# Performance work log

Measured on AMD Instinct MI355X. Metric: run time of the kernel, lower is better.

## Reference

```python
import jax, jax.numpy as jnp
import numpy as np

N_NODES = 50000
N_EDGES = 800000
IN_CH = 64
HID_CH = 128
OUT_CH = 64
N_GRAPHS = 512


def setup_inputs() -> dict:
    key = jax.random.key(0)
    ks = jax.random.split(key, 10)
    x = jax.random.normal(ks[0], (N_NODES, IN_CH), dtype=jnp.float32)
    edge_index = jax.random.randint(ks[1], (2, N_EDGES), 0, N_NODES, dtype=jnp.int64)
    batch = jnp.sort(jax.random.randint(ks[2], (N_NODES,), 0, N_GRAPHS, dtype=jnp.int64))
    s = 1.0 / np.sqrt(IN_CH)
    # SAGEConv (mean aggr): lin_l applied to aggregated neighbors (with bias),
    # lin_r applied to root features (no bias).
    W_l = jax.random.uniform(ks[3], (HID_CH, IN_CH), minval=-s, maxval=s, dtype=jnp.float32)
    b_l = jax.random.uniform(ks[4], (HID_CH,), minval=-s, maxval=s, dtype=jnp.float32)
    W_r = jax.random.uniform(ks[5], (HID_CH, IN_CH), minval=-s, maxval=s, dtype=jnp.float32)
    sh = 1.0 / np.sqrt(HID_CH)
    W_att = jax.random.uniform(ks[6], (1, HID_CH), minval=-sh, maxval=sh, dtype=jnp.float32)
    b_att = jax.random.uniform(ks[7], (1,), minval=-sh, maxval=sh, dtype=jnp.float32)
    W_out = jax.random.uniform(ks[8], (OUT_CH, HID_CH), minval=-sh, maxval=sh, dtype=jnp.float32)
    b_out = jax.random.uniform(ks[9], (OUT_CH,), minval=-sh, maxval=sh, dtype=jnp.float32)
    return {"x": x, "edge_index": edge_index, "batch": batch,
            "W_l": W_l, "b_l": b_l, "W_r": W_r,
            "W_att": W_att, "b_att": b_att, "W_out": W_out, "b_out": b_out}


def reference(x, edge_index, batch, W_l, b_l, W_r, W_att, b_att, W_out, b_out):
    src, dst = edge_index[0], edge_index[1]
    # mean aggregation of neighbor (source) features at each target node
    agg = jax.ops.segment_sum(x[src], dst, num_segments=N_NODES)  # [N, IN]
    deg = jax.ops.segment_sum(jnp.ones((N_EDGES,), x.dtype), dst, num_segments=N_NODES)
    agg = agg / jnp.maximum(deg, 1.0)[:, None]
    # SAGEConv: lin_l(aggr) + lin_r(x), then ReLU
    h = jax.nn.relu(agg @ W_l.T + b_l + x @ W_r.T)  # [N, HID]
    # attention weighting
    scores = jax.nn.sigmoid(h @ W_att.T + b_att)  # [N, 1]
    h = h * scores
    # global mean pool per graph
    pooled = jax.ops.segment_sum(h, batch, num_segments=N_GRAPHS)  # [B, HID]
    counts = jax.ops.segment_sum(jnp.ones((N_NODES,), x.dtype), batch, num_segments=N_GRAPHS)
    pooled = pooled / jnp.maximum(counts, 1.0)[:, None]
    return pooled @ W_out.T + b_out  # [B, OUT]
```

## Files before the change

kernel.cpp:

```cpp
#include <hip/hip_runtime.h>
#include <hip/hip_bf16.h>

#define N_NODES 50000
#define N_EDGES 800000
#define IN_CH 64
#define HID_CH 128
#define OUT_CH 64
#define N_GRAPHS 512
#define CAP 64
#define TN 16
#define NPB 64
#define NSTAGE (NPB / TN)

__device__ __forceinline__ void atomAddF(float* p, float v) {
    unsafeAtomicAdd(p, v);
}

#define PIN4(v) asm volatile("" : "+v"(v.x), "+v"(v.y), "+v"(v.z), "+v"(v.w))


__global__ __launch_bounds__(256) void scatter_pad(
    const int* __restrict__ ei, int* __restrict__ degi,
    unsigned short* __restrict__ csr16)
{
    int e = blockIdx.x * 256 + threadIdx.x;
    if (e >= N_EDGES) return;
    int src = ei[e];
    int dst = ei[N_EDGES + e];
    int pos = atomicAdd(&degi[dst], 1);
    csr16[(dst << 6) + pos] = (unsigned short)src;
}

__global__ __launch_bounds__(256) void gather_kernel(
    const float* __restrict__ x, const unsigned short* __restrict__ csr16,
    const int* __restrict__ degi, float* __restrict__ agg)
{
    int wid  = (blockIdx.x * 256 + threadIdx.x) >> 6;
    int lane = threadIdx.x & 63;
    if (wid >= N_NODES) return;
    int d = degi[wid];
    const unsigned short* b = csr16 + ((size_t)wid << 6);
    int g  = lane >> 4;
    int c4 = lane & 15;
    float4 acc  = make_float4(0.f, 0.f, 0.f, 0.f);
    float4 acc2 = make_float4(0.f, 0.f, 0.f, 0.f);
    int i = g;
    for (; i + 4 < d; i += 8) {
        int s0 = b[i];
        int s1 = b[i + 4];
        float4 v0 = *reinterpret_cast<const float4*>(x + (size_t)s0 * IN_CH + c4 * 4);
        float4 v1 = *reinterpret_cast<const float4*>(x + (size_t)s1 * IN_CH + c4 * 4);
        acc.x  += v0.x; acc.y  += v0.y; acc.z  += v0.z; acc.w  += v0.w;
        acc2.x += v1.x; acc2.y += v1.y; acc2.z += v1.z; acc2.w += v1.w;
    }
    if (i < d) {
        int s0 = b[i];
        float4 v0 = *reinterpret_cast<const float4*>(x + (size_t)s0 * IN_CH + c4 * 4);
        acc.x += v0.x; acc.y += v0.y; acc.z += v0.z; acc.w += v0.w;
    }
    acc.x += acc2.x; acc.y += acc2.y; acc.z += acc2.z; acc.w += acc2.w;
    acc.x += __shfl_xor(acc.x, 16); acc.y += __shfl_xor(acc.y, 16);
    acc.z += __shfl_xor(acc.z, 16); acc.w += __shfl_xor(acc.w, 16);
    acc.x += __shfl_xor(acc.x, 32); acc.y += __shfl_xor(acc.y, 32);
    acc.z += __shfl_xor(acc.z, 32); acc.w += __shfl_xor(acc.w, 32);
    if (g == 0) {
        float inv = 1.0f / fmaxf((float)d, 1.0f);
        acc.x *= inv; acc.y *= inv; acc.z *= inv; acc.w *= inv;
        *reinterpret_cast<float4*>(agg + (size_t)wid * IN_CH + c4 * 4) = acc;
    }
}

__global__ __launch_bounds__(256, 4) void node_kernel(
    const float* __restrict__ x, const float* __restrict__ agg,
    const int* __restrict__ batch,
    const float* __restrict__ Wl, const float* __restrict__ bl,
    const float* __restrict__ Wr, const float* __restrict__ Watt,
    const float* __restrict__ batt,
    float* __restrict__ pooled, float* __restrict__ counts)
{
    const int t    = threadIdx.x;
    const int jp   = t & 31;
    const int q    = t >> 5;
    const int w    = t >> 6;
    const int lane = t & 63;

    float4 wrk[4][2], wlk[4][2];
#pragma unroll
    for (int k = 0; k < 4; ++k) {
#pragma unroll
        for (int h = 0; h < 2; ++h) {
            wrk[k][h] = *reinterpret_cast<const float4*>(
                Wr + (size_t)(jp + 32 * k) * IN_CH + q * 8 + h * 4);
            wlk[k][h] = *reinterpret_cast<const float4*>(
                Wl + (size_t)(jp + 32 * k) * IN_CH + q * 8 + h * 4);
            PIN4(wrk[k][h]);
            PIN4(wlk[k][h]);
        }
    }
    const int jj    = t & 127;
    const float blj = bl[jj];
    const float wa  = Watt[jj];
    const float ba  = batt[0];

    __shared__ __align__(16) float4 feat[TN][32];
    float* sh = reinterpret_cast<float*>(feat);
    __shared__ float psum[4][TN][HID_CH];
    __shared__ float sred[2][TN];
    __shared__ float ss[TN];

    float accp = 0.f, cnt = 0.f;
    const int nb0 = blockIdx.x * NPB;
    int curb = batch[nb0];

    for (int s = 0; s < NSTAGE; ++s) {
        const int nb = nb0 + s * TN;
        if (nb >= N_NODES) break;
        __syncthreads();
#pragma unroll
        for (int k = 0; k < 2; ++k) {
            int f    = t + k * 256;
            int node = nb + (f >> 5);
            int slot = f & 31;
            const float* src = (slot < 16)
                ? x   + (size_t)node * IN_CH + slot * 4
                : agg + (size_t)node * IN_CH + (slot - 16) * 4;
            feat[f >> 5][slot] = *reinterpret_cast<const float4*>(src);
        }
        __syncthreads();

#pragma unroll
        for (int n = 0; n < TN; ++n) {
            float4 x0 = feat[n][2 * q];
            float4 x1 = feat[n][2 * q + 1];
            float4 a0 = feat[n][16 + 2 * q];
            float4 a1 = feat[n][16 + 2 * q + 1];
            float p[4];
#pragma unroll
            for (int k = 0; k < 4; ++k) {
                float e0 = wrk[k][0].x * x0.x + wrk[k][0].y * x0.y
                         + wrk[k][0].z * x0.z + wrk[k][0].w * x0.w;
                float e1 = wrk[k][1].x * x1.x + wrk[k][1].y * x1.y
                         + wrk[k][1].z * x1.z + wrk[k][1].w * x1.w;
                float e2 = wlk[k][0].x * a0.x + wlk[k][0].y * a0.y
                         + wlk[k][0].z * a0.z + wlk[k][0].w * a0.w;
                float e3 = wlk[k][1].x * a1.x + wlk[k][1].y * a1.y
                         + wlk[k][1].z * a1.z + wlk[k][1].w * a1.w;
                p[k] = (e0 + e1) + (e2 + e3);
            }
#pragma unroll
            for (int k = 0; k < 4; ++k)
                p[k] += __shfl_xor(p[k], 32);
            if (lane < 32) {
                psum[w][n][jp]      = p[0];
                psum[w][n][jp + 32] = p[1];
                psum[w][n][jp + 64] = p[2];
                psum[w][n][jp + 96] = p[3];
            }
        }
        __syncthreads();

        if (t < 128) {
#pragma unroll
            for (int n = 0; n < TN; ++n) {
                float h = psum[0][n][jj] + psum[1][n][jj]
                        + psum[2][n][jj] + psum[3][n][jj] + blj;
                h = fmaxf(h, 0.f);
                sh[n * HID_CH + jj] = h;
                float r = wa * h;
                r += __shfl_xor(r, 1);  r += __shfl_xor(r, 2);
                r += __shfl_xor(r, 4);  r += __shfl_xor(r, 8);
                r += __shfl_xor(r, 16); r += __shfl_xor(r, 32);
                if (lane == n) sred[t >> 6][n] = r;
            }
        }
        __syncthreads();
        if (t < TN) ss[t] = 1.f / (1.f + expf(-(sred[0][t] + sred[1][t] + ba)));
        __syncthreads();

        if (t < 128) {
#pragma unroll
            for (int n = 0; n < TN; ++n) {
                float hs = sh[n * HID_CH + jj] * ss[n];
                int b = batch[nb + n];
                if (b != curb) {
                    atomAddF(&pooled[(size_t)curb * HID_CH + jj], accp);
                    if (jj == 0) atomAddF(&counts[curb], cnt);
                    accp = 0.f; cnt = 0.f; curb = b;
                }
                accp += hs;
                cnt  += 1.f;
            }
        }
    }
    if (t < 128) {
        atomAddF(&pooled[(size_t)curb * HID_CH + jj], accp);
        if (jj == 0) atomAddF(&counts[curb], cnt);
    }
}

__global__ __launch_bounds__(64) void out_kernel(
    const float* __restrict__ pooled, const float* __restrict__ counts,
    const float* __restrict__ Wout, const float* __restrict__ bout,
    float* __restrict__ out)
{
    const int g = blockIdx.x;
    const int j = threadIdx.x;
    __shared__ __align__(16) float sp[HID_CH];
    float inv = 1.0f / fmaxf(counts[g], 1.0f);
    sp[j]      = pooled[(size_t)g * HID_CH + j] * inv;
    sp[j + 64] = pooled[(size_t)g * HID_CH + 64 + j] * inv;
    __syncthreads();
    float acc = bout[j];
#pragma unroll
    for (int c4 = 0; c4 < HID_CH / 4; ++c4) {
        float4 w = *reinterpret_cast<const float4*>(Wout + (size_t)j * HID_CH + c4 * 4);
        acc += w.x * sp[c4 * 4 + 0] + w.y * sp[c4 * 4 + 1]
             + w.z * sp[c4 * 4 + 2] + w.w * sp[c4 * 4 + 3];
    }
    out[(size_t)g * OUT_CH + j] = acc;
}

extern "C" void kernel_launch(void* const* d_in, const int* in_sizes, int n_in,
                              void* d_out, int out_size, void* d_ws, size_t ws_size,
                              hipStream_t stream)
{
    const float* x     = (const float*)d_in[0];
    const int*   ei    = (const int*)d_in[1];
    const int*   batch = (const int*)d_in[2];
    const float* Wl    = (const float*)d_in[3];
    const float* bl    = (const float*)d_in[4];
    const float* Wr    = (const float*)d_in[5];
    const float* Watt  = (const float*)d_in[6];
    const float* batt  = (const float*)d_in[7];
    const float* Wout  = (const float*)d_in[8];
    const float* bout  = (const float*)d_in[9];
    float* out = (float*)d_out;

    int*            degi   = (int*)d_ws;
    float*          pooled = (float*)(degi + N_NODES);
    float*          counts = pooled + (size_t)N_GRAPHS * HID_CH;
    unsigned short* csr16  = (unsigned short*)(counts + N_GRAPHS);
    float*          agg    = (float*)(csr16 + (size_t)N_NODES * CAP);

    size_t zero_bytes = ((size_t)N_NODES
                       + (size_t)N_GRAPHS * HID_CH + N_GRAPHS) * sizeof(int);
    hipMemsetAsync(d_ws, 0, zero_bytes, stream);

    scatter_pad<<<(N_EDGES + 255) / 256, 256, 0, stream>>>(ei, degi, csr16);
    gather_kernel<<<(N_NODES * 64 + 255) / 256, 256, 0, stream>>>(x, csr16, degi, agg);
    node_kernel<<<(N_NODES + NPB - 1) / NPB, 256, 0, stream>>>(
        x, agg, batch, Wl, bl, Wr, Watt, batt, pooled, counts);
    out_kernel<<<N_GRAPHS, 64, 0, stream>>>(pooled, counts, Wout, bout, out);
}
```

Baseline: 251.3 us.

## Remap node-kernel weight tiling, unroll gather 4-way, and double nodes per block

```diff
diff --git a/kernel.cpp b/kernel.cpp
--- a/kernel.cpp
+++ b/kernel.cpp
@@ -9,14 +9,12 @@
 #define N_GRAPHS 512
 #define CAP 64
 #define TN 16
-#define NPB 64
+#define NPB 128
 #define NSTAGE (NPB / TN)
 
 __device__ __forceinline__ void atomAddF(float* p, float v) {
     unsafeAtomicAdd(p, v);
 }
-
-#define PIN4(v) asm volatile("" : "+v"(v.x), "+v"(v.y), "+v"(v.z), "+v"(v.w))
 
 
 __global__ __launch_bounds__(256) void scatter_pad(
@@ -42,31 +40,44 @@
     const unsigned short* b = csr16 + ((size_t)wid << 6);
     int g  = lane >> 4;
     int c4 = lane & 15;
-    float4 acc  = make_float4(0.f, 0.f, 0.f, 0.f);
-    float4 acc2 = make_float4(0.f, 0.f, 0.f, 0.f);
+    float4 a0 = make_float4(0.f, 0.f, 0.f, 0.f);
+    float4 a1 = make_float4(0.f, 0.f, 0.f, 0.f);
+    float4 a2 = make_float4(0.f, 0.f, 0.f, 0.f);
+    float4 a3 = make_float4(0.f, 0.f, 0.f, 0.f);
     int i = g;
-    for (; i + 4 < d; i += 8) {
-        int s0 = b[i];
-        int s1 = b[i + 4];
+    for (; i + 12 < d; i += 16) {
+        int s0 = b[i], s1 = b[i + 4], s2 = b[i + 8], s3 = b[i + 12];
         float4 v0 = *reinterpret_cast<const float4*>(x + (size_t)s0 * IN_CH + c4 * 4);
         float4 v1 = *reinterpret_cast<const float4*>(x + (size_t)s1 * IN_CH + c4 * 4);
-        acc.x  += v0.x; acc.y  += v0.y; acc.z  += v0.z; acc.w  += v0.w;
-        acc2.x += v1.x; acc2.y += v1.y; acc2.z += v1.z; acc2.w += v1.w;
+        float4 v2 = *reinterpret_cast<const float4*>(x + (size_t)s2 * IN_CH + c4 * 4);
+        float4 v3 = *reinterpret_cast<const float4*>(x + (size_t)s3 * IN_CH + c4 * 4);
+        a0.x += v0.x; a0.y += v0.y; a0.z += v0.z; a0.w += v0.w;
+        a1.x += v1.x; a1.y += v1.y; a1.z += v1.z; a1.w += v1.w;
+        a2.x += v2.x; a2.y += v2.y; a2.z += v2.z; a2.w += v2.w;
+        a3.x += v3.x; a3.y += v3.y; a3.z += v3.z; a3.w += v3.w;
+    }
+    for (; i + 4 < d; i += 8) {
+        int s0 = b[i], s1 = b[i + 4];
+        float4 v0 = *reinterpret_cast<const float4*>(x + (size_t)s0 * IN_CH + c4 * 4);
+        float4 v1 = *reinterpret_cast<const float4*>(x + (size_t)s1 * IN_CH + c4 * 4);
+        a0.x += v0.x; a0.y += v0.y; a0.z += v0.z; a0.w += v0.w;
+        a1.x += v1.x; a1.y += v1.y; a1.z += v1.z; a1.w += v1.w;
     }
     if (i < d) {
         int s0 = b[i];
         float4 v0 = *reinterpret_cast<const float4*>(x + (size_t)s0 * IN_CH + c4 * 4);
-        acc.x += v0.x; acc.y += v0.y; acc.z += v0.z; acc.w += v0.w;
-    }
-    acc.x += acc2.x; acc.y += acc2.y; acc.z += acc2.z; acc.w += acc2.w;
-    acc.x += __shfl_xor(acc.x, 16); acc.y += __shfl_xor(acc.y, 16);
-    acc.z += __shfl_xor(acc.z, 16); acc.w += __shfl_xor(acc.w, 16);
-    acc.x += __shfl_xor(acc.x, 32); acc.y += __shfl_xor(acc.y, 32);
-    acc.z += __shfl_xor(acc.z, 32); acc.w += __shfl_xor(acc.w, 32);
+        a0.x += v0.x; a0.y += v0.y; a0.z += v0.z; a0.w += v0.w;
+    }
+    a0.x += a1.x + a2.x + a3.x; a0.y += a1.y + a2.y + a3.y;
+    a0.z += a1.z + a2.z + a3.z; a0.w += a1.w + a2.w + a3.w;
+    a0.x += __shfl_xor(a0.x, 16); a0.y += __shfl_xor(a0.y, 16);
+    a0.z += __shfl_xor(a0.z, 16); a0.w += __shfl_xor(a0.w, 16);
+    a0.x += __shfl_xor(a0.x, 32); a0.y += __shfl_xor(a0.y, 32);
+    a0.z += __shfl_xor(a0.z, 32); a0.w += __shfl_xor(a0.w, 32);
     if (g == 0) {
         float inv = 1.0f / fmaxf((float)d, 1.0f);
-        acc.x *= inv; acc.y *= inv; acc.z *= inv; acc.w *= inv;
-        *reinterpret_cast<float4*>(agg + (size_t)wid * IN_CH + c4 * 4) = acc;
+        a0.x *= inv; a0.y *= inv; a0.z *= inv; a0.w *= inv;
+        *reinterpret_cast<float4*>(agg + (size_t)wid * IN_CH + c4 * 4) = a0;
     }
 }
 
@@ -79,23 +90,17 @@
     float* __restrict__ pooled, float* __restrict__ counts)
 {
     const int t    = threadIdx.x;
-    const int jp   = t & 31;
-    const int q    = t >> 5;
-    const int w    = t >> 6;
+    const int jp   = t & 63;
+    const int q    = t >> 6;
     const int lane = t & 63;
 
-    float4 wrk[4][2], wlk[4][2];
-#pragma unroll
-    for (int k = 0; k < 4; ++k) {
-#pragma unroll
-        for (int h = 0; h < 2; ++h) {
-            wrk[k][h] = *reinterpret_cast<const float4*>(
-                Wr + (size_t)(jp + 32 * k) * IN_CH + q * 8 + h * 4);
-            wlk[k][h] = *reinterpret_cast<const float4*>(
-                Wl + (size_t)(jp + 32 * k) * IN_CH + q * 8 + h * 4);
-            PIN4(wrk[k][h]);
-            PIN4(wlk[k][h]);
-        }
+    float4 wl0[4], wl1[4], wr0[4], wr1[4];
+#pragma unroll
+    for (int c = 0; c < 4; ++c) {
+        wl0[c] = *reinterpret_cast<const float4*>(Wl + (size_t)jp * IN_CH + q * 16 + c * 4);
+        wr0[c] = *reinterpret_cast<const float4*>(Wr + (size_t)jp * IN_CH + q * 16 + c * 4);
+        wl1[c] = *reinterpret_cast<const float4*>(Wl + (size_t)(jp + 64) * IN_CH + q * 16 + c * 4);
+        wr1[c] = *reinterpret_cast<const float4*>(Wr + (size_t)(jp + 64) * IN_CH + q * 16 + c * 4);
     }
     const int jj    = t & 127;
     const float blj = bl[jj];
@@ -130,32 +135,22 @@
 
 #pragma unroll
         for (int n = 0; n < TN; ++n) {
-            float4 x0 = feat[n][2 * q];
-            float4 x1 = feat[n][2 * q + 1];
-            float4 a0 = feat[n][16 + 2 * q];
-            float4 a1 = feat[n][16 + 2 * q + 1];
-            float p[4];
-#pragma unroll
-            for (int k = 0; k < 4; ++k) {
-                float e0 = wrk[k][0].x * x0.x + wrk[k][0].y * x0.y
-                         + wrk[k][0].z * x0.z + wrk[k][0].w * x0.w;
-                float e1 = wrk[k][1].x * x1.x + wrk[k][1].y * x1.y
-                         + wrk[k][1].z * x1.z + wrk[k][1].w * x1.w;
-                float e2 = wlk[k][0].x * a0.x + wlk[k][0].y * a0.y
-                         + wlk[k][0].z * a0.z + wlk[k][0].w * a0.w;
-                float e3 = wlk[k][1].x * a1.x + wlk[k][1].y * a1.y
-                         + wlk[k][1].z * a1.z + wlk[k][1].w * a1.w;
-                p[k] = (e0 + e1) + (e2 + e3);
+            float p0a = 0.f, p0b = 0.f, p1a = 0.f, p1b = 0.f;
+#pragma unroll
+            for (int c = 0; c < 4; ++c) {
+                float4 xv = feat[n][q * 4 + c];
+                float4 av = feat[n][16 + q * 4 + c];
+                p0a += wr0[c].x * xv.x + wr0[c].y * xv.y
+                     + wl0[c].x * av.x + wl0[c].y * av.y;
+                p0b += wr0[c].z * xv.z + wr0[c].w * xv.w
+                     + wl0[c].z * av.z + wl0[c].w * av.w;
+                p1a += wr1[c].x * xv.x + wr1[c].y * xv.y
+                     + wl1[c].x * av.x + wl1[c].y * av.y;
+                p1b += wr1[c].z * xv.z + wr1[c].w * xv.w
+                     + wl1[c].z * av.z + wl1[c].w * av.w;
             }
-#pragma unroll
-            for (int k = 0; k < 4; ++k)
-                p[k] += __shfl_xor(p[k], 32);
-            if (lane < 32) {
-                psum[w][n][jp]      = p[0];
-                psum[w][n][jp + 32] = p[1];
-                psum[w][n][jp + 64] = p[2];
-                psum[w][n][jp + 96] = p[3];
-            }
+            psum[q][n][jp]      = p0a + p0b;
+            psum[q][n][jp + 64] = p1a + p1b;
         }
         __syncthreads();
 
```

Result: faster. 238.9 us (-4.9%).
